# Kernel optimization log

Measured on AMD Instinct MI355X. Metric: run time of the kernel, lower is better.

Reference implementation:

```python
import jax, jax.numpy as jnp
import numpy as np

EPS = 1e-5
SLOPE = 0.01  # LeakyReLU default
C = 512
C2 = C // 2
B, D, W, H = 2, 16, 16, 16


def _leaky(x):
    return jnp.where(x >= 0, x, SLOPE * x)


def _bn_c(x, g, b, rm, rv):
    # per-channel BN (eval mode) over axis 1 of a (B,C,...) tensor
    shape = (1, -1) + (1,) * (x.ndim - 2)
    inv = jax.lax.rsqrt(rv + EPS)
    return (x - rm.reshape(shape)) * (inv * g).reshape(shape) + b.reshape(shape)


def _bn_s(x, g, b, rm, rv):
    # scalar-feature BatchNorm1d(1) in eval mode
    return (x - rm[0]) * (jax.lax.rsqrt(rv[0] + EPS) * g[0]) + b[0]


def setup_inputs() -> dict:
    key = jax.random.key(0)
    ks = jax.random.split(key, 8)
    s = 0.02
    inp = {
        'x': jax.random.normal(ks[0], (B, C, D, W, H), jnp.float32),
        'topo_prompt': jax.random.normal(ks[1], (D, W, H, 6), jnp.float32) * s,
        # edge_aggregation_func: Linear(6,1)+BN1d(1)
        'w_ea': jax.random.normal(ks[2], (1, 6), jnp.float32) * s,
        'b_ea': jnp.zeros((1,), jnp.float32),
        'g_ea': jnp.ones((1,), jnp.float32), 'be_ea': jnp.zeros((1,), jnp.float32),
        'rm_ea': jnp.zeros((1,), jnp.float32), 'rv_ea': jnp.ones((1,), jnp.float32),
        # vertex_update_func: Linear(2C, C/2)+BN1d(C/2)
        'w_v': jax.random.normal(ks[3], (C2, 2 * C), jnp.float32) * s,
        'b_v': jnp.zeros((C2,), jnp.float32),
        'g_v': jnp.ones((C2,), jnp.float32), 'be_v': jnp.zeros((C2,), jnp.float32),
        'rm_v': jnp.zeros((C2,), jnp.float32), 'rv_v': jnp.ones((C2,), jnp.float32),
        # edge_update_func: Linear(2C, C/2)+BN1d(C/2)
        'w_e': jax.random.normal(ks[4], (C2, 2 * C), jnp.float32) * s,
        'b_e': jnp.zeros((C2,), jnp.float32),
        'g_e': jnp.ones((C2,), jnp.float32), 'be_e': jnp.zeros((C2,), jnp.float32),
        'rm_e': jnp.zeros((C2,), jnp.float32), 'rv_e': jnp.ones((C2,), jnp.float32),
        # update_edge_reduce_func: Linear(6,1)+BN1d(1)
        'w_r': jax.random.normal(ks[5], (1, 6), jnp.float32) * s,
        'b_r': jnp.zeros((1,), jnp.float32),
        'g_r': jnp.ones((1,), jnp.float32), 'be_r': jnp.zeros((1,), jnp.float32),
        'rm_r': jnp.zeros((1,), jnp.float32), 'rv_r': jnp.ones((1,), jnp.float32),
        # final_aggregation_layer: Conv3d(3C/2 -> C, k=1, bias=False)+BN3d(C)
        'w_f': jax.random.normal(ks[6], (C, C + C2), jnp.float32) * s,
        'g_f': jnp.ones((C,), jnp.float32), 'be_f': jnp.zeros((C,), jnp.float32),
        'rm_f': jnp.zeros((C,), jnp.float32), 'rv_f': jnp.ones((C,), jnp.float32),
    }
    return inp


def reference(x, topo_prompt,
              w_ea, b_ea, g_ea, be_ea, rm_ea, rv_ea,
              w_v, b_v, g_v, be_v, rm_v, rv_v,
              w_e, b_e, g_e, be_e, rm_e, rv_e,
              w_r, b_r, g_r, be_r, rm_r, rv_r,
              w_f, g_f, be_f, rm_f, rv_f):
    # 6-neighbor circular shifts: cat((x[-1:], x[:-1])) == roll(+1); cat((x[1:], x[:1])) == roll(-1)
    shifts = jnp.stack([
        jnp.roll(x, 1, axis=2), jnp.roll(x, -1, axis=2),
        jnp.roll(x, 1, axis=3), jnp.roll(x, -1, axis=3),
        jnp.roll(x, 1, axis=4), jnp.roll(x, -1, axis=4),
    ], axis=-1)  # (B,C,D,W,H,6)
    edge = shifts * x[..., None] + topo_prompt  # topo_prompt (D,W,H,6) broadcasts

    # edge aggregation: Linear(6->1) + BN1d(1) + LeakyReLU
    agg = jnp.einsum('bcdwhk,k->bcdwh', edge, w_ea[0]) + b_ea[0]
    agg = _leaky(_bn_s(agg, g_ea, be_ea, rm_ea, rv_ea))  # (B,C,D,W,H)

    # vertex update: Linear(2C->C/2) + BN + LeakyReLU
    feat_v = jnp.concatenate([x, agg], axis=1)  # (B,2C,D,W,H)
    uv = jnp.einsum('bcdwh,oc->bodwh', feat_v, w_v) + b_v[None, :, None, None, None]
    uv = _leaky(_bn_c(uv, g_v, be_v, rm_v, rv_v))  # (B,C/2,D,W,H)

    # edge update: cat(vertex x6, edge) on channel dim -> Linear(2C->C/2) + BN + LeakyReLU
    vrep = jnp.broadcast_to(x[..., None], x.shape + (6,))
    feat_e = jnp.concatenate([vrep, edge], axis=1)  # (B,2C,D,W,H,6)
    ue = jnp.einsum('bcdwhk,oc->bodwhk', feat_e, w_e) + b_e[None, :, None, None, None, None]
    ue = _leaky(_bn_c(ue, g_e, be_e, rm_e, rv_e))  # (B,C/2,D,W,H,6)

    # reduce 6 neighbors: Linear(6->1) + BN1d(1) + LeakyReLU
    ur = jnp.einsum('bodwhk,k->bodwh', ue, w_r[0]) + b_r[0]
    ur = _leaky(_bn_s(ur, g_r, be_r, rm_r, rv_r))  # (B,C/2,D,W,H)

    update_feature = uv * ur

    # final 1x1x1 conv (bias=False) + BN3d + LeakyReLU
    fused = jnp.concatenate([x, update_feature], axis=1)  # (B,3C/2,D,W,H)
    out = jnp.einsum('bcdwh,oc->bodwh', fused, w_f)
    out = _leaky(_bn_c(out, g_f, be_f, rm_f, rv_f))
    return out
```

## Files before the change

### kernel.cpp

```cpp
#include <hip/hip_runtime.h>

#define BATCH 2
#define C 512
#define C2 256
#define V 4096
#define NROWS 8192
#define EPS 1e-5f
#define SLOPE 0.01f
#define BPAD 40

typedef __bf16 bf16;
typedef __bf16 bf16x8 __attribute__((ext_vector_type(8)));
typedef __bf16 bf16x4 __attribute__((ext_vector_type(4)));
typedef float  f32x4  __attribute__((ext_vector_type(4)));

__device__ __forceinline__ float leaky(float x) { return x >= 0.f ? x : SLOPE * x; }

__device__ __forceinline__ int nbr(int v, int k) {
    int h = v & 15, w = (v >> 4) & 15, d = v >> 8;
    switch (k) {
        case 0: return (v & 0x0FF) | (((d + 15) & 15) << 8);
        case 1: return (v & 0x0FF) | (((d + 1) & 15) << 8);
        case 2: return (v & 0xF0F) | (((w + 15) & 15) << 4);
        case 3: return (v & 0xF0F) | (((w + 1) & 15) << 4);
        case 4: return (v & 0xFF0) | ((h + 15) & 15);
        default: return (v & 0xFF0) | ((h + 1) & 15);
    }
}

__device__ __forceinline__ void gload16(const bf16* g, bf16* l) {
    __builtin_amdgcn_global_load_lds(
        (const __attribute__((address_space(1))) void*)g,
        (__attribute__((address_space(3))) void*)l, 16, 0, 0);
}

__device__ __forceinline__ void stage_gl(bf16* buf, const bf16* srcbase, size_t ld,
                                         int kcol, int wv, int lane) {
    #pragma unroll
    for (int j = 0; j < 2; j++) {
        const int rl = wv * 32 + j * 16;
        gload16(srcbase + (size_t)(rl + (lane >> 2)) * ld + kcol + (lane & 3) * 8,
                buf + rl * 32);
    }
}

template<int SA, int SB>
__device__ __forceinline__ void mmstep(const bf16* A, const bf16* B,
                                       f32x4 (&acc)[4][4], int abase, int bbase,
                                       int lr, int kg)
{
    bf16x8 af[4], bv[4];
    #pragma unroll
    for (int mb = 0; mb < 4; mb++)
        af[mb] = *(const bf16x8*)(A + (abase + mb * 16 + lr) * SA + kg * 8);
    #pragma unroll
    for (int nb = 0; nb < 4; nb++)
        bv[nb] = *(const bf16x8*)(B + (bbase + nb * 16 + lr) * SB + kg * 8);
    #pragma unroll
    for (int mb = 0; mb < 4; mb++)
        #pragma unroll
        for (int nb = 0; nb < 4; nb++)
            acc[mb][nb] = __builtin_amdgcn_mfma_f32_16x16x32_bf16(af[mb], bv[nb], acc[mb][nb], 0, 0, 0);
}

__global__ __launch_bounds__(256) void k_prep(
    const float* wv, const float* we, const float* wf,
    const float* w_ea, const float* b_ea, const float* g_ea, const float* be_ea,
    const float* rm_ea, const float* rv_ea,
    const float* b_v, const float* g_v, const float* be_v, const float* rm_v, const float* rv_v,
    const float* b_e, const float* g_e, const float* be_e, const float* rm_e, const float* rv_e,
    const float* w_r, const float* b_r, const float* g_r, const float* be_r,
    const float* rm_r, const float* rv_r,
    const float* g_f, const float* be_f, const float* rm_f, const float* rv_f,
    float* P, float* obv, float* obe, float* obf,
    bf16* wmain, bf16* we2, bf16* owf)
{
    int i = blockIdx.x * 256 + threadIdx.x;
    if (i < 524288) {
        int o = i >> 10, c = i & 1023;
        float val;
        if (o < 256) val = rsqrtf(rv_v[o] + EPS) * g_v[o] * wv[(size_t)o * 1024 + c];
        else {
            int oe = o - 256;
            val = (c < 512) ? rsqrtf(rv_e[oe] + EPS) * g_e[oe] * we[(size_t)oe * 1024 + c] : 0.f;
        }
        wmain[i] = (bf16)val;
    } else if (i < 655360) {
        int j = i - 524288; int o = j >> 9, c = j & 511;
        we2[j] = (bf16)(rsqrtf(rv_e[o] + EPS) * g_e[o] * we[(size_t)o * 1024 + 512 + c]);
    } else if (i < 1048576) {
        int j = i - 655360; int o = j / 768;
        owf[j] = (bf16)(rsqrtf(rv_f[o] + EPS) * g_f[o] * wf[j]);
    }
    if (blockIdx.x == 0) {
        int t = threadIdx.x;
        obf[t]       = be_f[t]       - rsqrtf(rv_f[t]       + EPS) * g_f[t]       * rm_f[t];
        obf[t + 256] = be_f[t + 256] - rsqrtf(rv_f[t + 256] + EPS) * g_f[t + 256] * rm_f[t + 256];
        float sv = rsqrtf(rv_v[t] + EPS) * g_v[t];
        obv[t] = sv * (b_v[t] - rm_v[t]) + be_v[t];
        float se = rsqrtf(rv_e[t] + EPS) * g_e[t];
        obe[t] = se * (b_e[t] - rm_e[t]) + be_e[t];
        if (t < 6) {
            float sa = rsqrtf(rv_ea[0] + EPS) * g_ea[0];
            P[t] = sa * w_ea[t];
            float sr = rsqrtf(rv_r[0] + EPS) * g_r[0];
            P[8 + t] = sr * w_r[t];
        }
        if (t == 6) {
            float sa = rsqrtf(rv_ea[0] + EPS) * g_ea[0];
            P[6] = sa * (b_ea[0] - rm_ea[0]) + be_ea[0];
            float sr = rsqrtf(rv_r[0] + EPS) * g_r[0];
            P[14] = sr * (b_r[0] - rm_r[0]) + be_r[0];
        }
    }
}

__global__ __launch_bounds__(256) void k_aggT(
    const float* __restrict__ x, const float* __restrict__ topo,
    const float* __restrict__ P,
    bf16* __restrict__ xT, bf16* __restrict__ aggT)
{
    __shared__ float T[64][65];
    const int t = threadIdx.x;
    const int b = blockIdx.z, ct = blockIdx.y * 64, vt = blockIdx.x * 64;
    const int cl = t >> 2;
    const int c  = ct + cl;
    const int vl0 = (t & 3) * 16;
    const int v0 = vt + vl0;
    const int w = (v0 >> 4) & 15, d = v0 >> 8;
    const float* xp = x + (((size_t)b * C + c) << 12);

    float xr[16], xd0[16], xd1[16], xw0[16], xw1[16];
    #pragma unroll
    for (int i = 0; i < 4; i++) {
        float4 a;
        a = ((const float4*)(xp + v0))[i];                        xr [4*i]=a.x; xr [4*i+1]=a.y; xr [4*i+2]=a.z; xr [4*i+3]=a.w;
        a = ((const float4*)(xp + (((d+15)&15)<<8) + (w<<4)))[i]; xd0[4*i]=a.x; xd0[4*i+1]=a.y; xd0[4*i+2]=a.z; xd0[4*i+3]=a.w;
        a = ((const float4*)(xp + (((d+ 1)&15)<<8) + (w<<4)))[i]; xd1[4*i]=a.x; xd1[4*i+1]=a.y; xd1[4*i+2]=a.z; xd1[4*i+3]=a.w;
        a = ((const float4*)(xp + (d<<8) + (((w+15)&15)<<4)))[i]; xw0[4*i]=a.x; xw0[4*i+1]=a.y; xw0[4*i+2]=a.z; xw0[4*i+3]=a.w;
        a = ((const float4*)(xp + (d<<8) + (((w+ 1)&15)<<4)))[i]; xw1[4*i]=a.x; xw1[4*i+1]=a.y; xw1[4*i+2]=a.z; xw1[4*i+3]=a.w;
    }

    #pragma unroll
    for (int p = 0; p < 2; ++p) {
        float val[16];
        if (p == 0) {
            #pragma unroll
            for (int j = 0; j < 16; j++) val[j] = xr[j];
        } else {
            #pragma unroll
            for (int j = 0; j < 16; j++) {
                const float* tp = topo + (size_t)(v0 + j) * 6;
                float s = P[6];
                s = fmaf(P[0], fmaf(xd0[j], xr[j], tp[0]), s);
                s = fmaf(P[1], fmaf(xd1[j], xr[j], tp[1]), s);
                s = fmaf(P[2], fmaf(xw0[j], xr[j], tp[2]), s);
                s = fmaf(P[3], fmaf(xw1[j], xr[j], tp[3]), s);
                s = fmaf(P[4], fmaf(xr[(j+15)&15], xr[j], tp[4]), s);
                s = fmaf(P[5], fmaf(xr[(j+ 1)&15], xr[j], tp[5]), s);
                val[j] = leaky(s);
            }
        }
        __syncthreads();
        #pragma unroll
        for (int j = 0; j < 16; j++) T[cl][vl0 + j] = val[j];
        __syncthreads();
        const int vr = t >> 2, c0 = (t & 3) * 16;
        bf16x8 lo, hi;
        #pragma unroll
        for (int i = 0; i < 8; i++) {
            lo[i] = (bf16)T[c0 + i][vr];
            hi[i] = (bf16)T[c0 + 8 + i][vr];
        }
        bf16* dst = (p == 0) ? xT : aggT;
        bf16* dp = dst + ((size_t)(b << 12) + vt + vr) * C + ct + c0;
        *(bf16x8*)dp = lo;
        *(bf16x8*)(dp + 8) = hi;
    }
}

template<bool MAIN>
__device__ __forceinline__ void gemm_body(
    int m0, int n0, int kk, int nsteps,
    const bf16* __restrict__ wA, size_t ldA,
    const bf16* __restrict__ xT, const bf16* __restrict__ aggT,
    const float* __restrict__ topo, const float* __restrict__ bvp,
    bf16* __restrict__ uvT, float* __restrict__ sxe, bf16* __restrict__ se,
    bf16 (*A)[128 * 32], bf16 (*B)[128 * BPAD])
{
    const int t = threadIdx.x, lane = t & 63;
    const int wv = t >> 6, wmi = wv >> 1, wni = wv & 1;
    const int lr = lane & 15, kg = lane >> 4;

    const bf16* wAb  = wA + (size_t)m0 * ldA;
    const bf16* xTb  = xT + (size_t)n0 * C;
    const bf16* agTb = aggT + (size_t)n0 * C;

    const int erow = t >> 1, ecol = (t & 1) * 16;
    const bf16* pBx = nullptr; const bf16* pB2 = nullptr; float tp = 0.f;
    if (!MAIN) {
        const int rB = n0 + erow;
        const int vvv = rB & 4095, bb = rB >> 12;
        pBx = xT + (size_t)rB * C + ecol;
        pB2 = xT + (size_t)((bb << 12) | nbr(vvv, kk)) * C + ecol;
        tp = topo[vvv * 6 + kk];
    }

    f32x4 acc[4][4];
    #pragma unroll
    for (int mb = 0; mb < 4; mb++)
        #pragma unroll
        for (int nb = 0; nb < 4; nb++) acc[mb][nb] = 0.f;

    uint4 b0, b1, n0r, n1r;
    auto issueB = [&](int s) {
        b0  = *(const uint4*)(pBx + s * 32);
        b1  = *(const uint4*)(pBx + s * 32 + 8);
        n0r = *(const uint4*)(pB2 + s * 32);
        n1r = *(const uint4*)(pB2 + s * 32 + 8);
    };
    auto commitB = [&](int buf) {
        bf16x8 xa0 = *(bf16x8*)&b0, xn0 = *(bf16x8*)&n0r;
        bf16x8 xa1 = *(bf16x8*)&b1, xn1 = *(bf16x8*)&n1r;
        bf16x8 e0, e1;
        #pragma unroll
        for (int i = 0; i < 8; i++) {
            e0[i] = (bf16)fmaf((float)xa0[i], (float)xn0[i], tp);
            e1[i] = (bf16)fmaf((float)xa1[i], (float)xn1[i], tp);
        }
        *(bf16x8*)(&B[buf][erow * BPAD + ecol])     = e0;
        *(bf16x8*)(&B[buf][erow * BPAD + ecol + 8]) = e1;
    };
    auto stageStep = [&](int buf, int s) {
        stage_gl(A[buf], wAb, ldA, s * 32, wv, lane);
        if (MAIN) {
            if (s < 16) stage_gl(B[buf], xTb, C, s * 32, wv, lane);
            else        stage_gl(B[buf], agTb, C, (s - 16) * 32, wv, lane);
        }
    };

    stageStep(0, 0);
    if (!MAIN) { issueB(0); commitB(0); if (nsteps > 1) issueB(1); }

    int cb = 0;
    #pragma unroll 1
    for (int s = 0; s < nsteps; ++s) {
        __syncthreads();
        if (s + 1 < nsteps) stageStep(cb ^ 1, s + 1);
        if (MAIN) mmstep<32, 32>(A[cb], B[cb], acc, wmi * 64, wni * 64, lr, kg);
        else      mmstep<32, BPAD>(A[cb], B[cb], acc, wmi * 64, wni * 64, lr, kg);
        if (!MAIN && s + 1 < nsteps) {
            commitB(cb ^ 1);
            if (s + 2 < nsteps) issueB(s + 2);
        }
        cb ^= 1;
    }

    if (MAIN) {
        if (m0 < 256) {
            #pragma unroll
            for (int mb = 0; mb < 4; mb++) {
                const int o = m0 + wmi * 64 + mb * 16 + kg * 4;
                f32x4 bv4 = *(const f32x4*)(bvp + o);
                #pragma unroll
                for (int nb = 0; nb < 4; nb++) {
                    const int col = n0 + wni * 64 + nb * 16 + lr;
                    bf16x4 o4;
                    #pragma unroll
                    for (int q = 0; q < 4; q++)
                        o4[q] = (bf16)leaky(acc[mb][nb][q] + bv4[q]);
                    *(bf16x4*)(uvT + (size_t)col * C2 + o) = o4;
                }
            }
        } else {
            #pragma unroll
            for (int mb = 0; mb < 4; mb++) {
                const int o = (m0 - 256) + wmi * 64 + mb * 16 + kg * 4;
                #pragma unroll
                for (int nb = 0; nb < 4; nb++) {
                    const int col = n0 + wni * 64 + nb * 16 + lr;
                    *(f32x4*)(sxe + (size_t)col * C2 + o) = acc[mb][nb];
                }
            }
        }
    } else {
        #pragma unroll
        for (int mb = 0; mb < 4; mb++) {
            const int o = m0 + wmi * 64 + mb * 16 + kg * 4;
            #pragma unroll
            for (int nb = 0; nb < 4; nb++) {
                const int col = n0 + wni * 64 + nb * 16 + lr;
                bf16x4 o4;
                #pragma unroll
                for (int q = 0; q < 4; q++) o4[q] = (bf16)acc[mb][nb][q];
                *(bf16x4*)(se + ((size_t)kk * NROWS + col) * C2 + o) = o4;
            }
        }
    }
}

__global__ __launch_bounds__(256, 3) void k_gemm(
    const bf16* __restrict__ xT, const bf16* __restrict__ aggT,
    const bf16* __restrict__ wm, const bf16* __restrict__ we2,
    const float* __restrict__ bvp, const float* __restrict__ topo,
    bf16* __restrict__ uvT, float* __restrict__ sxe, bf16* __restrict__ se)
{
    __shared__ __align__(16) bf16 A[2][128 * 32];
    __shared__ __align__(16) bf16 B[2][128 * BPAD];
    const int lb = (blockIdx.x & 7) * 128 + (blockIdx.x >> 3);
    const int n0 = (lb >> 4) * 128;
    const int sub = lb & 15;
    if (sub < 4) {
        const int m0 = sub * 128;
        const int nsteps = (m0 < 256) ? 32 : 16;
        gemm_body<true>(m0, n0, 0, nsteps, wm, 1024, xT, aggT, topo, bvp,
                        uvT, sxe, nullptr, A, B);
    } else {
        const int e = sub - 4;
        const int kk = e >> 1, m0 = (e & 1) * 128;
        gemm_body<false>(m0, n0, kk, 16, we2, 512, xT, aggT, topo, bvp,
                         nullptr, nullptr, se, A, B);
    }
}

__global__ __launch_bounds__(256) void k_comb(
    const float* __restrict__ sxe, const bf16* __restrict__ se,
    const bf16* __restrict__ uvT, const float* __restrict__ bep,
    const float* __restrict__ P, bf16* __restrict__ updT)
{
    const int g = blockIdx.x * 256 + threadIdx.x;
    const int row = g >> 5, o0 = (g & 31) * 8;
    const size_t base = (size_t)row * C2 + o0;

    f32x4 sx0 = *(const f32x4*)(sxe + base);
    f32x4 sx1 = *(const f32x4*)(sxe + base + 4);
    f32x4 be0 = *(const f32x4*)(bep + o0);
    f32x4 be1 = *(const f32x4*)(bep + o0 + 4);
    float ur[8] = {};
    #pragma unroll
    for (int k = 0; k < 6; k++) {
        bf16x8 s8 = *(const bf16x8*)(se + (size_t)k * NROWS * C2 + base);
        const float wrk = P[8 + k];
        #pragma unroll
        for (int i = 0; i < 4; i++) {
            ur[i]     = fmaf(wrk, leaky(sx0[i] + (float)s8[i]     + be0[i]), ur[i]);
            ur[i + 4] = fmaf(wrk, leaky(sx1[i] + (float)s8[i + 4] + be1[i]), ur[i + 4]);
        }
    }
    const float brp = P[14];
    bf16x8 uv8 = *(const bf16x8*)(uvT + base);
    bf16x8 o8;
    #pragma unroll
    for (int i = 0; i < 8; i++)
        o8[i] = (bf16)((float)uv8[i] * leaky(ur[i] + brp));
    *(bf16x8*)(updT + base) = o8;
}

__global__ __launch_bounds__(256, 3) void k_out(
    const bf16* __restrict__ xT, const bf16* __restrict__ updT,
    const bf16* __restrict__ wf, const float* __restrict__ bfp,
    float* __restrict__ out)
{
    __shared__ __align__(16) bf16 A[2][128 * 32];
    __shared__ __align__(16) bf16 B[2][128 * 32];
    const int t = threadIdx.x, lane = t & 63;
    const int wv = t >> 6, wmi = wv >> 1, wni = wv & 1;
    const int lr = lane & 15, kg = lane >> 4;
    const int lb = (blockIdx.x & 7) * 32 + (blockIdx.x >> 3);
    const int n0 = (lb >> 2) * 128, m0 = (lb & 3) * 128;

    const bf16* wAb = wf   + (size_t)m0 * 768;
    const bf16* xTb = xT   + (size_t)n0 * C;
    const bf16* uTb = updT + (size_t)n0 * C2;

    f32x4 acc[4][4];
    #pragma unroll
    for (int mb = 0; mb < 4; mb++)
        #pragma unroll
        for (int nb = 0; nb < 4; nb++) acc[mb][nb] = 0.f;

    auto stageStep = [&](int buf, int s) {
        stage_gl(A[buf], wAb, 768, s * 32, wv, lane);
        if (s < 16) stage_gl(B[buf], xTb, C, s * 32, wv, lane);
        else        stage_gl(B[buf], uTb, C2, (s - 16) * 32, wv, lane);
    };

    stageStep(0, 0);
    int cb = 0;
    #pragma unroll 1
    for (int s = 0; s < 24; ++s) {
        __syncthreads();
        if (s + 1 < 24) stageStep(cb ^ 1, s + 1);
        mmstep<32, 32>(A[cb], B[cb], acc, wmi * 64, wni * 64, lr, kg);
        cb ^= 1;
    }

    #pragma unroll
    for (int mb = 0; mb < 4; mb++) {
        const int o = m0 + wmi * 64 + mb * 16 + kg * 4;
        f32x4 bf4 = *(const f32x4*)(bfp + o);
        #pragma unroll
        for (int nb = 0; nb < 4; nb++) {
            const int col = n0 + wni * 64 + nb * 16 + lr;
            const int b = col >> 12, v = col & 4095;
            #pragma unroll
            for (int q = 0; q < 4; q++)
                out[(((size_t)b * C + o + q) << 12) + v] = leaky(acc[mb][nb][q] + bf4[q]);
        }
    }
}

extern "C" void kernel_launch(void* const* d_in, const int* in_sizes, int n_in,
                              void* d_out, int out_size, void* d_ws, size_t ws_size,
                              hipStream_t stream)
{
    const float* x    = (const float*)d_in[0];
    const float* topo = (const float*)d_in[1];
    const float* w_ea = (const float*)d_in[2];
    const float* b_ea = (const float*)d_in[3];
    const float* g_ea = (const float*)d_in[4];
    const float* be_ea= (const float*)d_in[5];
    const float* rm_ea= (const float*)d_in[6];
    const float* rv_ea= (const float*)d_in[7];
    const float* w_v  = (const float*)d_in[8];
    const float* b_v  = (const float*)d_in[9];
    const float* g_v  = (const float*)d_in[10];
    const float* be_v = (const float*)d_in[11];
    const float* rm_v = (const float*)d_in[12];
    const float* rv_v = (const float*)d_in[13];
    const float* w_e  = (const float*)d_in[14];
    const float* b_e  = (const float*)d_in[15];
    const float* g_e  = (const float*)d_in[16];
    const float* be_e = (const float*)d_in[17];
    const float* rm_e = (const float*)d_in[18];
    const float* rv_e = (const float*)d_in[19];
    const float* w_r  = (const float*)d_in[20];
    const float* b_r  = (const float*)d_in[21];
    const float* g_r  = (const float*)d_in[22];
    const float* be_r = (const float*)d_in[23];
    const float* rm_r = (const float*)d_in[24];
    const float* rv_r = (const float*)d_in[25];
    const float* w_f  = (const float*)d_in[26];
    const float* g_f  = (const float*)d_in[27];
    const float* be_f = (const float*)d_in[28];
    const float* rm_f = (const float*)d_in[29];
    const float* rv_f = (const float*)d_in[30];

    char* base = (char*)d_ws;
    size_t off = 0;
    auto take = [&](size_t bytes) { size_t r = off; off = (off + bytes + 255) & ~(size_t)255; return r; };
    float* P    = (float*)(base + take(64 * 4));
    float* bvp  = (float*)(base + take(256 * 4));
    float* bep  = (float*)(base + take(256 * 4));
    float* bfp  = (float*)(base + take(512 * 4));
    bf16*  wmp  = (bf16*)(base + take((size_t)524288 * 2));
    bf16*  we2p = (bf16*)(base + take((size_t)131072 * 2));
    bf16*  wfp  = (bf16*)(base + take((size_t)393216 * 2));
    bf16*  xT   = (bf16*)(base + take((size_t)NROWS * C * 2));
    bf16*  aggT = (bf16*)(base + take((size_t)NROWS * C * 2));
    bf16*  uvT  = (bf16*)(base + take((size_t)NROWS * C2 * 2));
    bf16*  updT = (bf16*)(base + take((size_t)NROWS * C2 * 2));
    float* sxe  = (float*)(base + take((size_t)NROWS * C2 * 4));
    bf16*  se   = (bf16*)(base + take((size_t)6 * NROWS * C2 * 2));

    k_prep<<<4096, 256, 0, stream>>>(
        w_v, w_e, w_f,
        w_ea, b_ea, g_ea, be_ea, rm_ea, rv_ea,
        b_v, g_v, be_v, rm_v, rv_v,
        b_e, g_e, be_e, rm_e, rv_e,
        w_r, b_r, g_r, be_r, rm_r, rv_r,
        g_f, be_f, rm_f, rv_f,
        P, bvp, bep, bfp, wmp, we2p, wfp);

    k_aggT<<<dim3(64, 8, 2), 256, 0, stream>>>(x, topo, P, xT, aggT);

    k_gemm<<<dim3(1024), 256, 0, stream>>>(xT, aggT, wmp, we2p, bvp, topo, uvT, sxe, se);
    k_comb<<<dim3(NROWS * C2 / 8 / 256), 256, 0, stream>>>(sxe, se, uvT, bep, P, updT);
    k_out<<<dim3(256), 256, 0, stream>>>(xT, updT, wfp, bfp, (float*)d_out);
}
```

Baseline: 100.7 us.

## Double GEMM K-tile to 64 with XOR-swizzled LDS layout

```diff
diff --git a/kernel.cpp b/kernel.cpp
--- a/kernel.cpp
+++ b/kernel.cpp
@@ -7,7 +7,6 @@
 #define NROWS 8192
 #define EPS 1e-5f
 #define SLOPE 0.01f
-#define BPAD 40
 
 typedef __bf16 bf16;
 typedef __bf16 bf16x8 __attribute__((ext_vector_type(8)));
@@ -34,33 +33,37 @@
         (__attribute__((address_space(3))) void*)l, 16, 0, 0);
 }
 
-__device__ __forceinline__ void stage_gl(bf16* buf, const bf16* srcbase, size_t ld,
-                                         int kcol, int wv, int lane) {
-    #pragma unroll
-    for (int j = 0; j < 2; j++) {
-        const int rl = wv * 32 + j * 16;
-        gload16(srcbase + (size_t)(rl + (lane >> 2)) * ld + kcol + (lane & 3) * 8,
-                buf + rl * 32);
-    }
-}
-
-template<int SA, int SB>
-__device__ __forceinline__ void mmstep(const bf16* A, const bf16* B,
-                                       f32x4 (&acc)[4][4], int abase, int bbase,
-                                       int lr, int kg)
-{
-    bf16x8 af[4], bv[4];
-    #pragma unroll
-    for (int mb = 0; mb < 4; mb++)
-        af[mb] = *(const bf16x8*)(A + (abase + mb * 16 + lr) * SA + kg * 8);
-    #pragma unroll
-    for (int nb = 0; nb < 4; nb++)
-        bv[nb] = *(const bf16x8*)(B + (bbase + nb * 16 + lr) * SB + kg * 8);
-    #pragma unroll
-    for (int mb = 0; mb < 4; mb++)
+__device__ __forceinline__ void stage_gl64(bf16* buf, const bf16* srcbase, size_t ld,
+                                           int kcol, int wv, int lane) {
+    const int sslot = ((lane & 7) ^ (lane >> 3)) * 8;
+    #pragma unroll
+    for (int j = 0; j < 4; j++) {
+        const int rl = wv * 32 + j * 8;
+        gload16(srcbase + (size_t)(rl + (lane >> 3)) * ld + kcol + sslot,
+                buf + rl * 64);
+    }
+}
+
+__device__ __forceinline__ void mmstep64(const bf16* A, const bf16* B,
+                                         f32x4 (&acc)[4][4], int abase, int bbase,
+                                         int lr, int kg)
+{
+    #pragma unroll
+    for (int sub = 0; sub < 2; sub++) {
+        const int slot = ((sub * 4 + kg) ^ (lr & 7)) * 8;
+        bf16x8 af[4], bv[4];
+        #pragma unroll
+        for (int mb = 0; mb < 4; mb++)
+            af[mb] = *(const bf16x8*)(A + (abase + mb * 16 + lr) * 64 + slot);
         #pragma unroll
         for (int nb = 0; nb < 4; nb++)
-            acc[mb][nb] = __builtin_amdgcn_mfma_f32_16x16x32_bf16(af[mb], bv[nb], acc[mb][nb], 0, 0, 0);
+            bv[nb] = *(const bf16x8*)(B + (bbase + nb * 16 + lr) * 64 + slot);
+        #pragma unroll
+        for (int mb = 0; mb < 4; mb++)
+            #pragma unroll
+            for (int nb = 0; nb < 4; nb++)
+                acc[mb][nb] = __builtin_amdgcn_mfma_f32_16x16x32_bf16(af[mb], bv[nb], acc[mb][nb], 0, 0, 0);
+    }
 }
 
 __global__ __launch_bounds__(256) void k_prep(
@@ -186,7 +189,7 @@
     const bf16* __restrict__ xT, const bf16* __restrict__ aggT,
     const float* __restrict__ topo, const float* __restrict__ bvp,
     bf16* __restrict__ uvT, float* __restrict__ sxe, bf16* __restrict__ se,
-    bf16 (*A)[128 * 32], bf16 (*B)[128 * BPAD])
+    bf16 (*A)[128 * 64], bf16 (*B)[128 * 64])
 {
     const int t = threadIdx.x, lane = t & 63;
     const int wv = t >> 6, wmi = wv >> 1, wni = wv & 1;
@@ -196,14 +199,18 @@
     const bf16* xTb  = xT + (size_t)n0 * C;
     const bf16* agTb = aggT + (size_t)n0 * C;
 
-    const int erow = t >> 1, ecol = (t & 1) * 16;
+    const int erow = t >> 1, ecol = (t & 1) * 32;
     const bf16* pBx = nullptr; const bf16* pB2 = nullptr; float tp = 0.f;
+    int eslot[4];
     if (!MAIN) {
         const int rB = n0 + erow;
         const int vvv = rB & 4095, bb = rB >> 12;
         pBx = xT + (size_t)rB * C + ecol;
         pB2 = xT + (size_t)((bb << 12) | nbr(vvv, kk)) * C + ecol;
         tp = topo[vvv * 6 + kk];
+        #pragma unroll
+        for (int j = 0; j < 4; j++)
+            eslot[j] = ((((t & 1) * 4 + j) ^ (erow & 7)) * 8);
     }
 
     f32x4 acc[4][4];
@@ -212,30 +219,30 @@
         #pragma unroll
         for (int nb = 0; nb < 4; nb++) acc[mb][nb] = 0.f;
 
-    uint4 b0, b1, n0r, n1r;
+    uint4 bx[4], bn[4];
     auto issueB = [&](int s) {
-        b0  = *(const uint4*)(pBx + s * 32);
-        b1  = *(const uint4*)(pBx + s * 32 + 8);
-        n0r = *(const uint4*)(pB2 + s * 32);
-        n1r = *(const uint4*)(pB2 + s * 32 + 8);
+        #pragma unroll
+        for (int j = 0; j < 4; j++) {
+            bx[j] = *(const uint4*)(pBx + s * 64 + j * 8);
+            bn[j] = *(const uint4*)(pB2 + s * 64 + j * 8);
+        }
     };
     auto commitB = [&](int buf) {
-        bf16x8 xa0 = *(bf16x8*)&b0, xn0 = *(bf16x8*)&n0r;
-        bf16x8 xa1 = *(bf16x8*)&b1, xn1 = *(bf16x8*)&n1r;
-        bf16x8 e0, e1;
-        #pragma unroll
-        for (int i = 0; i < 8; i++) {
-            e0[i] = (bf16)fmaf((float)xa0[i], (float)xn0[i], tp);
-            e1[i] = (bf16)fmaf((float)xa1[i], (float)xn1[i], tp);
-        }
-        *(bf16x8*)(&B[buf][erow * BPAD + ecol])     = e0;
-        *(bf16x8*)(&B[buf][erow * BPAD + ecol + 8]) = e1;
+        #pragma unroll
+        for (int j = 0; j < 4; j++) {
+            bf16x8 xa = *(bf16x8*)&bx[j], xn = *(bf16x8*)&bn[j];
+            bf16x8 e;
+            #pragma unroll
+            for (int i = 0; i < 8; i++)
+                e[i] = (bf16)fmaf((float)xa[i], (float)xn[i], tp);
+            *(bf16x8*)(&B[buf][erow * 64 + eslot[j]]) = e;
+        }
     };
     auto stageStep = [&](int buf, int s) {
-        stage_gl(A[buf], wAb, ldA, s * 32, wv, lane);
+        stage_gl64(A[buf], wAb, ldA, s * 64, wv, lane);
         if (MAIN) {
-            if (s < 16) stage_gl(B[buf], xTb, C, s * 32, wv, lane);
-            else        stage_gl(B[buf], agTb, C, (s - 16) * 32, wv, lane);
+            const bf16* src = (s < 8) ? xTb : agTb;
+            stage_gl64(B[buf], src, C, (s & 7) * 64, wv, lane);
         }
     };
 
@@ -247,8 +254,7 @@
     for (int s = 0; s < nsteps; ++s) {
         __syncthreads();
         if (s + 1 < nsteps) stageStep(cb ^ 1, s + 1);
-        if (MAIN) mmstep<32, 32>(A[cb], B[cb], acc, wmi * 64, wni * 64, lr, kg);
-        else      mmstep<32, BPAD>(A[cb], B[cb], acc, wmi * 64, wni * 64, lr, kg);
+        mmstep64(A[cb], B[cb], acc, wmi * 64, wni * 64, lr, kg);
         if (!MAIN && s + 1 < nsteps) {
             commitB(cb ^ 1);
             if (s + 2 < nsteps) issueB(s + 2);
@@ -299,26 +305,26 @@
     }
 }
 
-__global__ __launch_bounds__(256, 3) void k_gemm(
+__global__ __launch_bounds__(256, 2) void k_gemm(
     const bf16* __restrict__ xT, const bf16* __restrict__ aggT,
     const bf16* __restrict__ wm, const bf16* __restrict__ we2,
     const float* __restrict__ bvp, const float* __restrict__ topo,
     bf16* __restrict__ uvT, float* __restrict__ sxe, bf16* __restrict__ se)
 {
-    __shared__ __align__(16) bf16 A[2][128 * 32];
-    __shared__ __align__(16) bf16 B[2][128 * BPAD];
+    __shared__ __align__(16) bf16 A[2][128 * 64];
+    __shared__ __align__(16) bf16 B[2][128 * 64];
     const int lb = (blockIdx.x & 7) * 128 + (blockIdx.x >> 3);
     const int n0 = (lb >> 4) * 128;
     const int sub = lb & 15;
     if (sub < 4) {
         const int m0 = sub * 128;
-        const int nsteps = (m0 < 256) ? 32 : 16;
+        const int nsteps = (m0 < 256) ? 16 : 8;
         gemm_body<true>(m0, n0, 0, nsteps, wm, 1024, xT, aggT, topo, bvp,
                         uvT, sxe, nullptr, A, B);
     } else {
         const int e = sub - 4;
         const int kk = e >> 1, m0 = (e & 1) * 128;
-        gemm_body<false>(m0, n0, kk, 16, we2, 512, xT, aggT, topo, bvp,
+        gemm_body<false>(m0, n0, kk, 8, we2, 512, xT, aggT, topo, bvp,
                          nullptr, nullptr, se, A, B);
     }
 }
@@ -356,13 +362,13 @@
     *(bf16x8*)(updT + base) = o8;
 }
 
-__global__ __launch_bounds__(256, 3) void k_out(
+__global__ __launch_bounds__(256, 2) void k_out(
     const bf16* __restrict__ xT, const bf16* __restrict__ updT,
     const bf16* __restrict__ wf, const float* __restrict__ bfp,
     float* __restrict__ out)
 {
-    __shared__ __align__(16) bf16 A[2][128 * 32];
-    __shared__ __align__(16) bf16 B[2][128 * 32];
+    __shared__ __align__(16) bf16 A[2][128 * 64];
+    __shared__ __align__(16) bf16 B[2][128 * 64];
     const int t = threadIdx.x, lane = t & 63;
     const int wv = t >> 6, wmi = wv >> 1, wni = wv & 1;
     const int lr = lane & 15, kg = lane >> 4;
@@ -380,18 +386,18 @@
         for (int nb = 0; nb < 4; nb++) acc[mb][nb] = 0.f;
 
     auto stageStep = [&](int buf, int s) {
-        stage_gl(A[buf], wAb, 768, s * 32, wv, lane);
-        if (s < 16) stage_gl(B[buf], xTb, C, s * 32, wv, lane);
-        else        stage_gl(B[buf], uTb, C2, (s - 16) * 32, wv, lane);
+        stage_gl64(A[buf], wAb, 768, s * 64, wv, lane);
+        if (s < 8) stage_gl64(B[buf], xTb, C, s * 64, wv, lane);
+        else       stage_gl64(B[buf], uTb, C2, (s - 8) * 64, wv, lane);
     };
 
     stageStep(0, 0);
     int cb = 0;
     #pragma unroll 1
-    for (int s = 0; s < 24; ++s) {
+    for (int s = 0; s < 12; ++s) {
         __syncthreads();
-        if (s + 1 < 24) stageStep(cb ^ 1, s + 1);
-        mmstep<32, 32>(A[cb], B[cb], acc, wmi * 64, wni * 64, lr, kg);
+        if (s + 1 < 12) stageStep(cb ^ 1, s + 1);
+        mmstep64(A[cb], B[cb], acc, wmi * 64, wni * 64, lr, kg);
         cb ^= 1;
     }
 
```

Measured after the change: 96.05 us. -4.6%, faster.
